# Optimization experiments

Measured on AMD Instinct MI355X. Metric: run time of the kernel, lower is better.

## Reference

```python
import jax, jax.numpy as jnp
import numpy as np

N_NODES = 50000
N_EDGES = 600000
IN_DIM = 64
HIDDEN = 128
N_REL = 10
N_LAYERS = 6
N_GRAPHS = 64
LN_EPS = 1e-5


def setup_inputs() -> dict:
    key = jax.random.key(0)
    ks = jax.random.split(key, 12)
    x = jax.random.normal(ks[0], (N_NODES, IN_DIM), dtype=jnp.float32)
    edge_index = jax.random.randint(ks[1], (2, N_EDGES), 0, N_NODES, dtype=jnp.int32)
    edge_type = jax.random.randint(ks[2], (N_EDGES,), 0, N_REL, dtype=jnp.int32)
    batch = jnp.sort(jax.random.randint(ks[3], (N_NODES,), 0, N_GRAPHS, dtype=jnp.int32))
    s_in = 1.0 / np.sqrt(IN_DIM)
    s_h = 1.0 / np.sqrt(HIDDEN)
    Wp = jax.random.uniform(ks[4], (IN_DIM, HIDDEN), jnp.float32, -s_in, s_in)
    bp = jax.random.uniform(ks[5], (HIDDEN,), jnp.float32, -s_in, s_in)
    rel_w = jax.random.uniform(ks[6], (N_LAYERS, N_REL, HIDDEN, HIDDEN), jnp.float32, -s_h, s_h)
    root_w = jax.random.uniform(ks[7], (N_LAYERS, HIDDEN, HIDDEN), jnp.float32, -s_h, s_h)
    conv_b = jnp.zeros((N_LAYERS, HIDDEN), jnp.float32)
    ln_g = jnp.ones((N_LAYERS, HIDDEN), jnp.float32)
    ln_b = jnp.zeros((N_LAYERS, HIDDEN), jnp.float32)
    return {"x": x, "edge_index": edge_index, "edge_type": edge_type, "batch": batch,
            "Wp": Wp, "bp": bp, "rel_w": rel_w, "root_w": root_w, "conv_b": conv_b,
            "ln_g": ln_g, "ln_b": ln_b}


def _layer_norm(h, g, b):
    mu = jnp.mean(h, axis=-1, keepdims=True)
    var = jnp.mean(jnp.square(h - mu), axis=-1, keepdims=True)
    return (h - mu) * jax.lax.rsqrt(var + LN_EPS) * g + b


def _rgcn_conv(h, src, dst, etype, Wr, Wroot, b):
    # PyG RGCNConv (aggr='mean'): out_i = x_i @ root + bias + sum_r mean_{j in N_r(i)} x_j @ W_r
    out = h @ Wroot + b
    hs = h[src]  # [E, H] gathered messages (relation-agnostic, transform after aggregation)
    for r in range(N_REL):
        m = (etype == r)
        msg = jnp.where(m[:, None], hs, 0.0)
        s = jax.ops.segment_sum(msg, dst, num_segments=N_NODES)
        cnt = jax.ops.segment_sum(m.astype(h.dtype), dst, num_segments=N_NODES)
        agg = s / jnp.maximum(cnt, 1.0)[:, None]
        out = out + agg @ Wr[r]
    return out


def reference(x, edge_index, edge_type, batch, Wp, bp, rel_w, root_w, conv_b, ln_g, ln_b):
    src, dst = edge_index[0], edge_index[1]
    h = x @ Wp + bp
    for l in range(N_LAYERS):
        residual = h
        h = _rgcn_conv(h, src, dst, edge_type, rel_w[l], root_w[l], conv_b[l])
        h = _layer_norm(h, ln_g[l], ln_b[l])
        h = jax.nn.relu(h)
        # dropout: identity in eval mode
        h = h + residual
    return jax.ops.segment_sum(h, batch, num_segments=N_GRAPHS)  # global_add_pool -> [G, H]
```

## Files before the change

kernel.cpp:

```cpp
#include <hip/hip_runtime.h>

#define NN 50000
#define NE 600000
#define IND 64
#define HID 128
#define NREL 10
#define NLAY 6
#define NG 64
#define LN_EPS 1e-5f
#define NMAT 11

typedef __attribute__((ext_vector_type(8))) short bf8;
typedef __attribute__((ext_vector_type(4))) float f4;

__device__ __forceinline__ ushort f2bf(float x) {
  uint u = __float_as_uint(x);
  u += 0x7fff + ((u >> 16) & 1);
  return (ushort)(u >> 16);
}
__device__ __forceinline__ float bf2f(ushort h) {
  return __uint_as_float(((uint)h) << 16);
}

__global__ void zero_kernel(float* __restrict__ p, int n) {
  int i = blockIdx.x * blockDim.x + threadIdx.x;
  int stride = gridDim.x * blockDim.x;
  for (; i < n; i += stride) p[i] = 0.f;
}

__global__ void count_edges(const int* __restrict__ dst, const int* __restrict__ et,
                            float* __restrict__ winv, int* __restrict__ deg) {
  int e = blockIdx.x * 256 + threadIdx.x;
  if (e >= NE) return;
  int d = dst[e];
  atomicAdd(&winv[d * NREL + et[e]], 1.0f);
  atomicAdd(&deg[d], 1);
}

__global__ void invert_winv(float* __restrict__ winv) {
  int i = blockIdx.x * 256 + threadIdx.x;
  if (i < NN * NREL) winv[i] = 1.0f / fmaxf(winv[i], 1.0f);
}

__global__ void scan_block(const int* __restrict__ deg, int* __restrict__ rowstart,
                           int* __restrict__ partial) {
  __shared__ int sh[256];
  int i = blockIdx.x * 256 + threadIdx.x;
  int v = (i < NN) ? deg[i] : 0;
  sh[threadIdx.x] = v;
  __syncthreads();
  int x = v;
  for (int off = 1; off < 256; off <<= 1) {
    int y = (threadIdx.x >= off) ? sh[threadIdx.x - off] : 0;
    __syncthreads();
    x += y;
    sh[threadIdx.x] = x;
    __syncthreads();
  }
  if (i < NN) rowstart[i] = x - v;
  if (threadIdx.x == 255) partial[blockIdx.x] = x;
}

__global__ void scan_partials(int* __restrict__ partial, int nb) {
  __shared__ int sh[256];
  int v = (threadIdx.x < nb) ? partial[threadIdx.x] : 0;
  sh[threadIdx.x] = v;
  __syncthreads();
  int x = v;
  for (int off = 1; off < 256; off <<= 1) {
    int y = (threadIdx.x >= off) ? sh[threadIdx.x - off] : 0;
    __syncthreads();
    x += y;
    sh[threadIdx.x] = x;
    __syncthreads();
  }
  partial[threadIdx.x] = x - v;
}

__global__ void scan_add(int* __restrict__ rowstart, const int* __restrict__ partial) {
  int i = blockIdx.x * 256 + threadIdx.x;
  if (i < NN) rowstart[i] += partial[i >> 8];
  if (i == 0) rowstart[NN] = NE;
}

__global__ void fill_csr(const int* __restrict__ dst, const int* __restrict__ src,
                         const int* __restrict__ et, int* __restrict__ fillpos,
                         const int* __restrict__ rowstart, const float* __restrict__ winv,
                         int* __restrict__ pkd, float* __restrict__ wsc) {
  int e = blockIdx.x * 256 + threadIdx.x;
  if (e >= NE) return;
  int d = dst[e], t = et[e];
  int pos = rowstart[d] + atomicAdd(&fillpos[d], 1);
  pkd[pos] = (src[e] << 4) | t;
  wsc[pos] = winv[d * NREL + t];
}

__global__ void transpose_split_frag(const float* __restrict__ src, ushort* __restrict__ dh,
                                     ushort* __restrict__ dl, int nmat, int K,
                                     int ddiv, int dmul, int dadd) {
  int i = blockIdx.x * 256 + threadIdx.x;
  int tot = nmat * K * 128;
  if (i >= tot) return;
  int m = i / (K * 128);
  int rem = i - m * (K * 128);
  int k = rem / 128;
  int n = rem - k * 128;
  float v = src[i];
  ushort h = f2bf(v);
  int dm = (m / ddiv) * dmul + (m % ddiv) + dadd;
  size_t o = (size_t)dm * (K * 128) + (size_t)(n >> 4) * (K * 16) + (k >> 3) * 128 +
             (n & 15) * 8 + (k & 7);
  dh[o] = h;
  dl[o] = f2bf(v - bf2f(h));
}

template <int K>
__global__ __launch_bounds__(256) void split_frag(const float* __restrict__ src,
                                                  ushort* __restrict__ dh,
                                                  ushort* __restrict__ dl) {
  constexpr int TOT = 16 * K;
  __shared__ ushort sh[TOT], sl[TOT];
  int grp = blockIdx.x;
  const float* s = src + (size_t)grp * TOT;
  for (int i = threadIdx.x * 4; i < TOT; i += 1024) {
    float4 v = *(const float4*)(s + i);
    int nl = i / K, d = i - nl * K;
    int off = (d >> 3) * 128 + nl * 8 + (d & 7);
    ushort h0 = f2bf(v.x), h1 = f2bf(v.y), h2 = f2bf(v.z), h3 = f2bf(v.w);
    *(uint*)(sh + off) = (uint)h0 | ((uint)h1 << 16);
    *(uint*)(sh + off + 2) = (uint)h2 | ((uint)h3 << 16);
    *(uint*)(sl + off) = (uint)f2bf(v.x - bf2f(h0)) | ((uint)f2bf(v.y - bf2f(h1)) << 16);
    *(uint*)(sl + off + 2) = (uint)f2bf(v.z - bf2f(h2)) | ((uint)f2bf(v.w - bf2f(h3)) << 16);
  }
  __syncthreads();
  size_t base = (size_t)grp * TOT;
  for (int i = threadIdx.x * 8; i < TOT; i += 2048) {
    *(bf8*)(dh + base + i) = *(const bf8*)(sh + i);
    *(bf8*)(dl + base + i) = *(const bf8*)(sl + i);
  }
}

struct Frags {
  bf8 ah[4], al[4], bh[4], bl[4];
};

template <int K>
__device__ __forceinline__ void load_frags(Frags& f, int ks, const ushort* Abh,
                                           const ushort* Abl, const ushort* Bbh,
                                           const ushort* Bbl) {
#pragma unroll
  for (int m = 0; m < 4; ++m) {
    f.ah[m] = *(const bf8*)(Abh + (size_t)m * (K * 16) + ks * 512);
    f.al[m] = *(const bf8*)(Abl + (size_t)m * (K * 16) + ks * 512);
  }
#pragma unroll
  for (int n = 0; n < 4; ++n) {
    f.bh[n] = *(const bf8*)(Bbh + (size_t)n * (K * 16) + ks * 512);
    f.bl[n] = *(const bf8*)(Bbl + (size_t)n * (K * 16) + ks * 512);
  }
}

__device__ __forceinline__ void mfma_frags(f4 (&acc)[4][4], const Frags& f) {
#pragma unroll
  for (int m = 0; m < 4; ++m)
#pragma unroll
    for (int n = 0; n < 4; ++n) {
      acc[m][n] = __builtin_amdgcn_mfma_f32_16x16x32_bf16(f.ah[m], f.bh[n], acc[m][n], 0, 0, 0);
      acc[m][n] = __builtin_amdgcn_mfma_f32_16x16x32_bf16(f.al[m], f.bh[n], acc[m][n], 0, 0, 0);
      acc[m][n] = __builtin_amdgcn_mfma_f32_16x16x32_bf16(f.ah[m], f.bl[n], acc[m][n], 0, 0, 0);
    }
}

template <int K>
__global__ __launch_bounds__(256) void gemm_frag(
    const ushort* __restrict__ Ah, const ushort* __restrict__ Al,
    const ushort* __restrict__ Bh, const ushort* __restrict__ Bl,
    const float* __restrict__ bias, float* __restrict__ Cf, ushort* __restrict__ Cb,
    int ldc, int M, int nrel) {
  int nwg = gridDim.x * gridDim.y;
  int lin = blockIdx.y * gridDim.x + blockIdx.x;
  int q = nwg >> 3, r8 = nwg & 7;
  int xcd = lin & 7, sub = lin >> 3;
  int swz = (xcd < r8) ? (xcd * (q + 1) + sub) : (r8 * (q + 1) + (xcd - r8) * q + sub);
  int bx = swz % gridDim.x;
  int by = swz / gridDim.x;

  const int bm = by * 128;
  const int tid = threadIdx.x, w = tid >> 6, lane = tid & 63;
  const int wr = (w >> 1) * 64, wc = (w & 1) * 64;
  const int lr = lane & 15;

  const ushort* Abh = Ah + ((size_t)(bm >> 4) + (wr >> 4)) * (K * 16) + lane * 8;
  const ushort* Abl = Al + ((size_t)(bm >> 4) + (wr >> 4)) * (K * 16) + lane * 8;
  const ushort* Bbh = Bh + (size_t)bx * (128 * K) + (size_t)(wc >> 4) * (K * 16) + lane * 8;
  const ushort* Bbl = Bl + (size_t)bx * (128 * K) + (size_t)(wc >> 4) * (K * 16) + lane * 8;

  f4 acc[4][4] = {};
  Frags fa, fb;
  if constexpr (K == 64) {
    load_frags<K>(fa, 0, Abh, Abl, Bbh, Bbl);
    load_frags<K>(fb, 1, Abh, Abl, Bbh, Bbl);
    mfma_frags(acc, fa);
    mfma_frags(acc, fb);
  } else {
    load_frags<K>(fa, 0, Abh, Abl, Bbh, Bbl);
    load_frags<K>(fb, 1, Abh, Abl, Bbh, Bbl);
    mfma_frags(acc, fa);
    load_frags<K>(fa, 2, Abh, Abl, Bbh, Bbl);
    mfma_frags(acc, fb);
    load_frags<K>(fb, 3, Abh, Abl, Bbh, Bbl);
    mfma_frags(acc, fa);
    mfma_frags(acc, fb);
  }

  const bool isroot = (bx == nrel);
  const int rgrp = (lane >> 4) * 4;
#pragma unroll
  for (int n = 0; n < 4; ++n) {
    int col = wc + n * 16 + lr;
    float bv = isroot ? bias[col] : 0.f;
#pragma unroll
    for (int m = 0; m < 4; ++m) {
      int r0 = bm + wr + m * 16 + rgrp;
#pragma unroll
      for (int j = 0; j < 4; ++j) {
        int r = r0 + j;
        if (r < M) {
          float v = acc[m][n][j];
          if (isroot) Cf[(size_t)r * 128 + col] = v + bv;
          else Cb[(size_t)r * ldc + bx * 128 + col] = f2bf(v);
        }
      }
    }
  }
}

__global__ __launch_bounds__(256) void aggregate(
    const int* __restrict__ pkd, const float* __restrict__ wsc,
    const int* __restrict__ rowstart, const ushort* __restrict__ T,
    float* __restrict__ OUT, int r0, int G) {
  int node = blockIdx.x * 4 + (threadIdx.x >> 6);
  if (node >= NN) return;
  int lane = threadIdx.x & 63;
  int e0 = rowstart[node], e1 = rowstart[node + 1];
  const int TW = G * HID;
  const int lo = lane * 2;
  float ax = 0.f, ay = 0.f;
  int p = e0;
  constexpr int U = 8;
  for (; p + U <= e1; p += U) {
    int pk[U];
    float wg[U];
    size_t ad[U];
#pragma unroll
    for (int u = 0; u < U; ++u) {
      pk[u] = pkd[p + u];
      wg[u] = wsc[p + u];
    }
#pragma unroll
    for (int u = 0; u < U; ++u) {
      int t = (pk[u] & 15) - r0;
      bool ok = (unsigned)t < (unsigned)G;
      ad[u] = ok ? ((size_t)(pk[u] >> 4) * TW + t * HID) : 0;
      if (!ok) wg[u] = 0.f;
    }
    uint v[U];
#pragma unroll
    for (int u = 0; u < U; ++u) v[u] = *(const uint*)(T + ad[u] + lo);
#pragma unroll
    for (int u = 0; u < U; ++u) {
      ax += wg[u] * bf2f((ushort)(v[u] & 0xffffu));
      ay += wg[u] * bf2f((ushort)(v[u] >> 16));
    }
  }
  for (; p < e1; ++p) {
    int pk = pkd[p];
    float wg = wsc[p];
    int t = (pk & 15) - r0;
    if ((unsigned)t < (unsigned)G) {
      uint v = *(const uint*)(T + (size_t)(pk >> 4) * TW + t * HID + lo);
      ax += wg * bf2f((ushort)(v & 0xffffu));
      ay += wg * bf2f((ushort)(v >> 16));
    }
  }
  float2* o = (float2*)(OUT + (size_t)node * HID + lo);
  float2 cur = *o;
  cur.x += ax;
  cur.y += ay;
  *o = cur;
}

__global__ __launch_bounds__(256) void ln_relu_res_frag(
    const float* __restrict__ OUT, float* __restrict__ h,
    const float* __restrict__ g, const float* __restrict__ b,
    ushort* __restrict__ dh, ushort* __restrict__ dl) {
  __shared__ ushort sh[2048], sl[2048];
  int grp = blockIdx.x;
  int w = threadIdx.x >> 6, lane = threadIdx.x & 63;
  float2 gg = *(const float2*)(g + lane * 2);
  float2 bb = *(const float2*)(b + lane * 2);
#pragma unroll
  for (int p = 0; p < 4; ++p) {
    int r = w * 4 + p;
    int node = grp * 16 + r;
    float2 v = *(const float2*)(OUT + (size_t)node * HID + lane * 2);
    float s = v.x + v.y, sq = v.x * v.x + v.y * v.y;
#pragma unroll
    for (int off = 32; off; off >>= 1) {
      s += __shfl_xor(s, off);
      sq += __shfl_xor(sq, off);
    }
    float mu = s * (1.f / HID);
    float var = sq * (1.f / HID) - mu * mu;
    float rs = rsqrtf(var + LN_EPS);
    float2 rr = *(const float2*)(h + (size_t)node * HID + lane * 2);
    float y0 = fmaxf((v.x - mu) * rs * gg.x + bb.x, 0.f) + rr.x;
    float y1 = fmaxf((v.y - mu) * rs * gg.y + bb.y, 0.f) + rr.y;
    *(float2*)(h + (size_t)node * HID + lane * 2) = make_float2(y0, y1);
    int d = lane * 2;
    int off2 = (d >> 3) * 128 + r * 8 + (d & 7);
    ushort h0 = f2bf(y0), h1 = f2bf(y1);
    *(uint*)(sh + off2) = (uint)h0 | ((uint)h1 << 16);
    *(uint*)(sl + off2) =
        (uint)f2bf(y0 - bf2f(h0)) | ((uint)f2bf(y1 - bf2f(h1)) << 16);
  }
  __syncthreads();
  size_t base = (size_t)grp * 2048;
  int t8 = threadIdx.x * 8;
  *(bf8*)(dh + base + t8) = *(const bf8*)(sh + t8);
  *(bf8*)(dl + base + t8) = *(const bf8*)(sl + t8);
}

__global__ void pool_kernel(const float* __restrict__ h, const int* __restrict__ batch,
                            float* __restrict__ out) {
  int n0 = blockIdx.x * 64;
  if (n0 >= NN) return;
  int t = threadIdx.x;
  int nend = min(n0 + 64, NN);
  int cur = batch[n0];
  float acc = 0.f;
  for (int n = n0; n < nend; ++n) {
    int gph = batch[n];
    if (gph != cur) {
      atomicAdd(&out[cur * HID + t], acc);
      acc = 0.f;
      cur = gph;
    }
    acc += h[(size_t)n * HID + t];
  }
  atomicAdd(&out[cur * HID + t], acc);
}

extern "C" void kernel_launch(void* const* d_in, const int* in_sizes, int n_in,
                              void* d_out, int out_size, void* d_ws, size_t ws_size,
                              hipStream_t stream) {
  const float* x = (const float*)d_in[0];
  const int* ei = (const int*)d_in[1];
  const int* et = (const int*)d_in[2];
  const int* batch = (const int*)d_in[3];
  const float* Wp = (const float*)d_in[4];
  const float* bp = (const float*)d_in[5];
  const float* rel_w = (const float*)d_in[6];
  const float* root_w = (const float*)d_in[7];
  const float* conv_b = (const float*)d_in[8];
  const float* ln_g = (const float*)d_in[9];
  const float* ln_b = (const float*)d_in[10];
  float* out = (float*)d_out;
  const int* srcv = ei;
  const int* dstv = ei + NE;

  const int NGRP = NN / 16;
  const int NGRP_PAD = NGRP + 3;

  char* w = (char*)d_ws;
  auto alloc = [&](size_t bytes) {
    char* p = w;
    w += (bytes + 255) & ~(size_t)255;
    return p;
  };
  float* h = (float*)alloc((size_t)NN * HID * 4);
  float* OUT = (float*)alloc((size_t)NN * HID * 4);
  float* winv = (float*)alloc((size_t)NN * NREL * 4);
  int* deg = (int*)alloc((size_t)NN * 4);
  int* rowstart = (int*)alloc((size_t)(NN + 1) * 4);
  int* fillpos = (int*)alloc((size_t)NN * 4);
  int* pkd = (int*)alloc((size_t)NE * 4);
  float* wsc = (float*)alloc((size_t)NE * 4);
  int* partial = (int*)alloc(256 * 4);
  ushort* xh = (ushort*)alloc((size_t)NGRP_PAD * 1024 * 2);
  ushort* xl = (ushort*)alloc((size_t)NGRP_PAD * 1024 * 2);
  ushort* hh = (ushort*)alloc((size_t)NGRP_PAD * 2048 * 2);
  ushort* hl = (ushort*)alloc((size_t)NGRP_PAD * 2048 * 2);
  ushort* Wph = (ushort*)alloc((size_t)IND * HID * 2);
  ushort* Wpl = (ushort*)alloc((size_t)IND * HID * 2);
  ushort* Relh = (ushort*)alloc((size_t)NLAY * NMAT * HID * HID * 2);
  ushort* Rell = (ushort*)alloc((size_t)NLAY * NMAT * HID * HID * 2);

  size_t used = (size_t)(w - (char*)d_ws);
  size_t rem = (ws_size > used) ? ws_size - used : 0;
  int G = 1;
  if (rem >= (size_t)NN * 10 * HID * 2) G = 10;
  else if (rem >= (size_t)NN * 5 * HID * 2) G = 5;
  else if (rem >= (size_t)NN * 2 * HID * 2) G = 2;
  ushort* T = (ushort*)alloc((size_t)NN * G * HID * 2);
  const int P = NREL / G;

  const int NB_E = (NE + 255) / 256;
  const int NB_N = (NN + 255) / 256;
  const int MB = (NN + 127) / 128;

  zero_kernel<<<dim3(512), dim3(256), 0, stream>>>(winv, NN * NREL);
  zero_kernel<<<dim3(256), dim3(256), 0, stream>>>((float*)deg, NN);
  zero_kernel<<<dim3(256), dim3(256), 0, stream>>>((float*)fillpos, NN);
  zero_kernel<<<dim3(32), dim3(256), 0, stream>>>(out, NG * HID);

  count_edges<<<dim3(NB_E), dim3(256), 0, stream>>>(dstv, et, winv, deg);
  invert_winv<<<dim3((NN * NREL + 255) / 256), dim3(256), 0, stream>>>(winv);
  scan_block<<<dim3(NB_N), dim3(256), 0, stream>>>(deg, rowstart, partial);
  scan_partials<<<dim3(1), dim3(256), 0, stream>>>(partial, NB_N);
  scan_add<<<dim3(NB_N), dim3(256), 0, stream>>>(rowstart, partial);
  fill_csr<<<dim3(NB_E), dim3(256), 0, stream>>>(dstv, srcv, et, fillpos, rowstart,
                                                 winv, pkd, wsc);

  transpose_split_frag<<<dim3((IND * HID + 255) / 256), dim3(256), 0, stream>>>(
      Wp, Wph, Wpl, 1, IND, 1, 1, 0);
  transpose_split_frag<<<dim3((NLAY * NREL * HID * HID + 255) / 256), dim3(256), 0, stream>>>(
      rel_w, Relh, Rell, NLAY * NREL, HID, NREL, NMAT, 0);
  transpose_split_frag<<<dim3((NLAY * HID * HID + 255) / 256), dim3(256), 0, stream>>>(
      root_w, Relh, Rell, NLAY, HID, 1, NMAT, NREL);

  split_frag<IND><<<dim3(NGRP), dim3(256), 0, stream>>>(x, xh, xl);

  gemm_frag<IND><<<dim3(1, MB), dim3(256), 0, stream>>>(
      xh, xl, Wph, Wpl, bp, h, (ushort*)nullptr, 128, NN, 0);
  split_frag<HID><<<dim3(NGRP), dim3(256), 0, stream>>>(h, hh, hl);

  for (int l = 0; l < NLAY; ++l) {
    const ushort* Bh = Relh + (size_t)l * NMAT * HID * HID;
    const ushort* Bl = Rell + (size_t)l * NMAT * HID * HID;
    if (G == NREL) {
      gemm_frag<HID><<<dim3(NREL + 1, MB), dim3(256), 0, stream>>>(
          hh, hl, Bh, Bl, conv_b + (size_t)l * HID, OUT, T, G * HID, NN, NREL);
      aggregate<<<dim3(NN / 4), dim3(256), 0, stream>>>(pkd, wsc, rowstart, T, OUT, 0, G);
    } else {
      gemm_frag<HID><<<dim3(1, MB), dim3(256), 0, stream>>>(
          hh, hl, Bh + (size_t)NREL * HID * HID, Bl + (size_t)NREL * HID * HID,
          conv_b + (size_t)l * HID, OUT, (ushort*)nullptr, 128, NN, 0);
      for (int p = 0; p < P; ++p) {
        gemm_frag<HID><<<dim3(G, MB), dim3(256), 0, stream>>>(
            hh, hl, Bh + (size_t)p * G * HID * HID, Bl + (size_t)p * G * HID * HID,
            (const float*)nullptr, (float*)nullptr, T, G * HID, NN, -1);
        aggregate<<<dim3(NN / 4), dim3(256), 0, stream>>>(pkd, wsc, rowstart, T, OUT,
                                                          p * G, G);
      }
    }
    ln_relu_res_frag<<<dim3(NGRP), dim3(256), 0, stream>>>(
        OUT, h, ln_g + (size_t)l * HID, ln_b + (size_t)l * HID, hh, hl);
  }

  pool_kernel<<<dim3((NN + 63) / 64), dim3(128), 0, stream>>>(h, batch, out);
}
```

Baseline: 1.084 ms.

## Fuse aggregation with layernorm and stage GEMM bf16 output through LDS

Adds an agg_ln kernel that performs the neighbour aggregation and the layernorm/relu/residual in one pass. This avoids writing OUT back to memory and launching a separate LN kernel, and it skips the split write on the last layer. The GEMM epilogue for relation outputs now stages bf16 tiles in shared memory so the global stores are coalesced 16-byte writes. The three zero kernels are also merged into one launch over the contiguous buffer. The costs are 34KB of LDS per GEMM block, which may lower occupancy, and one aggregation block per 16 nodes instead of per 4.

```diff
diff --git a/kernel.cpp b/kernel.cpp
--- a/kernel.cpp
+++ b/kernel.cpp
@@ -177,6 +177,7 @@
     const ushort* __restrict__ Bh, const ushort* __restrict__ Bl,
     const float* __restrict__ bias, float* __restrict__ Cf, ushort* __restrict__ Cb,
     int ldc, int M, int nrel) {
+  __shared__ ushort st[128][136];
   int nwg = gridDim.x * gridDim.y;
   int lin = blockIdx.y * gridDim.x + blockIdx.x;
   int q = nwg >> 3, r8 = nwg & 7;
@@ -213,25 +214,120 @@
     mfma_frags(acc, fb);
   }
 
-  const bool isroot = (bx == nrel);
   const int rgrp = (lane >> 4) * 4;
-#pragma unroll
-  for (int n = 0; n < 4; ++n) {
-    int col = wc + n * 16 + lr;
-    float bv = isroot ? bias[col] : 0.f;
-#pragma unroll
-    for (int m = 0; m < 4; ++m) {
-      int r0 = bm + wr + m * 16 + rgrp;
-#pragma unroll
-      for (int j = 0; j < 4; ++j) {
-        int r = r0 + j;
-        if (r < M) {
-          float v = acc[m][n][j];
-          if (isroot) Cf[(size_t)r * 128 + col] = v + bv;
-          else Cb[(size_t)r * ldc + bx * 128 + col] = f2bf(v);
+  if (bx == nrel) {
+#pragma unroll
+    for (int n = 0; n < 4; ++n) {
+      int col = wc + n * 16 + lr;
+      float bv = bias[col];
+#pragma unroll
+      for (int m = 0; m < 4; ++m) {
+        int r0 = bm + wr + m * 16 + rgrp;
+#pragma unroll
+        for (int j = 0; j < 4; ++j) {
+          int r = r0 + j;
+          if (r < M) Cf[(size_t)r * 128 + col] = acc[m][n][j] + bv;
         }
       }
     }
+  } else {
+#pragma unroll
+    for (int n = 0; n < 4; ++n) {
+      int col = wc + n * 16 + lr;
+#pragma unroll
+      for (int m = 0; m < 4; ++m) {
+        int r0 = wr + m * 16 + rgrp;
+#pragma unroll
+        for (int j = 0; j < 4; ++j) st[r0 + j][col] = f2bf(acc[m][n][j]);
+      }
+    }
+    __syncthreads();
+    const int rr = tid >> 4;
+    const int cc = (tid & 15) * 8;
+#pragma unroll
+    for (int it = 0; it < 8; ++it) {
+      int row = it * 16 + rr;
+      int grow = bm + row;
+      if (grow < M) {
+        bf8 v = *(const bf8*)&st[row][cc];
+        *(bf8*)(Cb + (size_t)grow * ldc + bx * 128 + cc) = v;
+      }
+    }
+  }
+}
+
+__global__ __launch_bounds__(256) void agg_ln(
+    const int* __restrict__ pkd, const float* __restrict__ wsc,
+    const int* __restrict__ rowstart, const ushort* __restrict__ T,
+    const float* __restrict__ OUT, float* __restrict__ h,
+    const float* __restrict__ g, const float* __restrict__ b,
+    ushort* __restrict__ dh, ushort* __restrict__ dl, int writeSplit) {
+  __shared__ ushort sh[2048], sl[2048];
+  const int grp = blockIdx.x;
+  const int w = threadIdx.x >> 6, lane = threadIdx.x & 63;
+  const int lo = lane * 2;
+  float2 gg = *(const float2*)(g + lo);
+  float2 bb = *(const float2*)(b + lo);
+  constexpr int TW = NREL * HID;
+#pragma unroll
+  for (int p4 = 0; p4 < 4; ++p4) {
+    int r = w * 4 + p4;
+    int node = grp * 16 + r;
+    float2 rt = *(const float2*)(OUT + (size_t)node * HID + lo);
+    float ax = 0.f, ay = 0.f;
+    int e0 = rowstart[node], e1 = rowstart[node + 1];
+    int p = e0;
+    constexpr int U = 8;
+    for (; p + U <= e1; p += U) {
+      int pk[U];
+      float wg[U];
+      uint v[U];
+#pragma unroll
+      for (int u = 0; u < U; ++u) {
+        pk[u] = pkd[p + u];
+        wg[u] = wsc[p + u];
+      }
+#pragma unroll
+      for (int u = 0; u < U; ++u)
+        v[u] = *(const uint*)(T + (size_t)(pk[u] >> 4) * TW + (pk[u] & 15) * HID + lo);
+#pragma unroll
+      for (int u = 0; u < U; ++u) {
+        ax += wg[u] * bf2f((ushort)(v[u] & 0xffffu));
+        ay += wg[u] * bf2f((ushort)(v[u] >> 16));
+      }
+    }
+    for (; p < e1; ++p) {
+      int pk = pkd[p];
+      float wg = wsc[p];
+      uint v = *(const uint*)(T + (size_t)(pk >> 4) * TW + (pk & 15) * HID + lo);
+      ax += wg * bf2f((ushort)(v & 0xffffu));
+      ay += wg * bf2f((ushort)(v >> 16));
+    }
+    float vx = rt.x + ax, vy = rt.y + ay;
+    float s = vx + vy, sq = vx * vx + vy * vy;
+#pragma unroll
+    for (int off = 32; off; off >>= 1) {
+      s += __shfl_xor(s, off);
+      sq += __shfl_xor(sq, off);
+    }
+    float mu = s * (1.f / HID);
+    float var = sq * (1.f / HID) - mu * mu;
+    float rs = rsqrtf(var + LN_EPS);
+    float2 rr2 = *(const float2*)(h + (size_t)node * HID + lo);
+    float y0 = fmaxf((vx - mu) * rs * gg.x + bb.x, 0.f) + rr2.x;
+    float y1 = fmaxf((vy - mu) * rs * gg.y + bb.y, 0.f) + rr2.y;
+    *(float2*)(h + (size_t)node * HID + lo) = make_float2(y0, y1);
+    int off2 = (lo >> 3) * 128 + r * 8 + (lo & 7);
+    ushort h0 = f2bf(y0), h1 = f2bf(y1);
+    *(uint*)(sh + off2) = (uint)h0 | ((uint)h1 << 16);
+    *(uint*)(sl + off2) = (uint)f2bf(y0 - bf2f(h0)) | ((uint)f2bf(y1 - bf2f(h1)) << 16);
+  }
+  __syncthreads();
+  if (writeSplit) {
+    size_t base = (size_t)grp * 2048;
+    int t8 = threadIdx.x * 8;
+    *(bf8*)(dh + base + t8) = *(const bf8*)(sh + t8);
+    *(bf8*)(dl + base + t8) = *(const bf8*)(sl + t8);
   }
 }
 
@@ -321,8 +417,7 @@
     int off2 = (d >> 3) * 128 + r * 8 + (d & 7);
     ushort h0 = f2bf(y0), h1 = f2bf(y1);
     *(uint*)(sh + off2) = (uint)h0 | ((uint)h1 << 16);
-    *(uint*)(sl + off2) =
-        (uint)f2bf(y0 - bf2f(h0)) | ((uint)f2bf(y1 - bf2f(h1)) << 16);
+    *(uint*)(sl + off2) = (uint)f2bf(y0 - bf2f(h0)) | ((uint)f2bf(y1 - bf2f(h1)) << 16);
   }
   __syncthreads();
   size_t base = (size_t)grp * 2048;
@@ -384,6 +479,7 @@
   int* deg = (int*)alloc((size_t)NN * 4);
   int* rowstart = (int*)alloc((size_t)(NN + 1) * 4);
   int* fillpos = (int*)alloc((size_t)NN * 4);
+  char* zend = w;
   int* pkd = (int*)alloc((size_t)NE * 4);
   float* wsc = (float*)alloc((size_t)NE * 4);
   int* partial = (int*)alloc(256 * 4);
@@ -408,10 +504,9 @@
   const int NB_E = (NE + 255) / 256;
   const int NB_N = (NN + 255) / 256;
   const int MB = (NN + 127) / 128;
-
-  zero_kernel<<<dim3(512), dim3(256), 0, stream>>>(winv, NN * NREL);
-  zero_kernel<<<dim3(256), dim3(256), 0, stream>>>((float*)deg, NN);
-  zero_kernel<<<dim3(256), dim3(256), 0, stream>>>((float*)fillpos, NN);
+  const int ZSPAN = (int)((zend - (char*)winv) / 4);
+
+  zero_kernel<<<dim3(1024), dim3(256), 0, stream>>>(winv, ZSPAN);
   zero_kernel<<<dim3(32), dim3(256), 0, stream>>>(out, NG * HID);
 
   count_edges<<<dim3(NB_E), dim3(256), 0, stream>>>(dstv, et, winv, deg);
@@ -441,7 +536,9 @@
     if (G == NREL) {
       gemm_frag<HID><<<dim3(NREL + 1, MB), dim3(256), 0, stream>>>(
           hh, hl, Bh, Bl, conv_b + (size_t)l * HID, OUT, T, G * HID, NN, NREL);
-      aggregate<<<dim3(NN / 4), dim3(256), 0, stream>>>(pkd, wsc, rowstart, T, OUT, 0, G);
+      agg_ln<<<dim3(NGRP), dim3(256), 0, stream>>>(
+          pkd, wsc, rowstart, T, OUT, h, ln_g + (size_t)l * HID, ln_b + (size_t)l * HID,
+          hh, hl, (l != NLAY - 1) ? 1 : 0);
     } else {
       gemm_frag<HID><<<dim3(1, MB), dim3(256), 0, stream>>>(
           hh, hl, Bh + (size_t)NREL * HID * HID, Bl + (size_t)NREL * HID * HID,
@@ -453,9 +550,9 @@
         aggregate<<<dim3(NN / 4), dim3(256), 0, stream>>>(pkd, wsc, rowstart, T, OUT,
                                                           p * G, G);
       }
-    }
-    ln_relu_res_frag<<<dim3(NGRP), dim3(256), 0, stream>>>(
-        OUT, h, ln_g + (size_t)l * HID, ln_b + (size_t)l * HID, hh, hl);
+      ln_relu_res_frag<<<dim3(NGRP), dim3(256), 0, stream>>>(
+          OUT, h, ln_g + (size_t)l * HID, ln_b + (size_t)l * HID, hh, hl);
+    }
   }
 
   pool_kernel<<<dim3((NN + 63) / 64), dim3(128), 0, stream>>>(h, batch, out);
```

New measurement: 909.4 us. 16.1% less time.

## Aggregate per-relation features before transform and fuse into one K=1536 GEMM

Applied to the files above, without the earlier changes.

Swaps the order of work: each layer now gathers bf16 node features per relation (mean-weighted) into a per-node 10x128 buffer, then runs one GEMM with concatenated K (root hi, root lo, 10 relation blocks) against a prepacked weight matrix. The old path computed ten per-relation transforms for every node and then gathered from that large transformed table. The new order removes the large intermediate T write and read and the multiple launches. In exchange the aggregated messages are bf16 with no low-part correction, and the root term drops the lo-by-lo product, which may cost accuracy. It also merges the zeroing launches and skips the split writes on the last layer.

```diff
diff --git a/kernel.cpp b/kernel.cpp
--- a/kernel.cpp
+++ b/kernel.cpp
@@ -8,7 +8,6 @@
 #define NLAY 6
 #define NG 64
 #define LN_EPS 1e-5f
-#define NMAT 11
 
 typedef __attribute__((ext_vector_type(8))) short bf8;
 typedef __attribute__((ext_vector_type(4))) float f4;
@@ -96,28 +95,54 @@
 }
 
 __global__ void transpose_split_frag(const float* __restrict__ src, ushort* __restrict__ dh,
-                                     ushort* __restrict__ dl, int nmat, int K,
-                                     int ddiv, int dmul, int dadd) {
+                                     ushort* __restrict__ dl, int K) {
   int i = blockIdx.x * 256 + threadIdx.x;
-  int tot = nmat * K * 128;
+  int tot = K * 128;
   if (i >= tot) return;
-  int m = i / (K * 128);
-  int rem = i - m * (K * 128);
-  int k = rem / 128;
-  int n = rem - k * 128;
+  int k = i / 128;
+  int n = i - k * 128;
   float v = src[i];
   ushort h = f2bf(v);
-  int dm = (m / ddiv) * dmul + (m % ddiv) + dadd;
-  size_t o = (size_t)dm * (K * 128) + (size_t)(n >> 4) * (K * 16) + (k >> 3) * 128 +
-             (n & 15) * 8 + (k & 7);
+  size_t o = (size_t)(n >> 4) * (K * 16) + (k >> 3) * 128 + (n & 15) * 8 + (k & 7);
   dh[o] = h;
   dl[o] = f2bf(v - bf2f(h));
+}
+
+__global__ void pack_B(const float* __restrict__ root_w, const float* __restrict__ rel_w,
+                       ushort* __restrict__ Bp) {
+  int i = blockIdx.x * 256 + threadIdx.x;
+  const int tot = NLAY * 1536 * 128;
+  if (i >= tot) return;
+  int l = i / (1536 * 128);
+  int rem = i - l * (1536 * 128);
+  int k = rem >> 7;
+  int n = rem & 127;
+  ushort s1, s2;
+  if (k < 128) {
+    float v = root_w[(size_t)l * 16384 + k * 128 + n];
+    s1 = f2bf(v);
+    s2 = f2bf(v - bf2f(s1));
+  } else if (k < 256) {
+    float v = root_w[(size_t)l * 16384 + (k - 128) * 128 + n];
+    s1 = f2bf(v);
+    s2 = 0;
+  } else {
+    int r = (k - 256) >> 7, kk = (k - 256) & 127;
+    float v = rel_w[(((size_t)l * NREL + r) * 128 + kk) * 128 + n];
+    s1 = f2bf(v);
+    s2 = f2bf(v - bf2f(s1));
+  }
+  size_t off = (size_t)(n >> 4) * 24576 + (k >> 3) * 128 + (n & 15) * 8 + (k & 7);
+  size_t base = (size_t)l * 2 * 196608;
+  Bp[base + off] = s1;
+  Bp[base + 196608 + off] = s2;
 }
 
 template <int K>
 __global__ __launch_bounds__(256) void split_frag(const float* __restrict__ src,
                                                   ushort* __restrict__ dh,
-                                                  ushort* __restrict__ dl) {
+                                                  ushort* __restrict__ dl,
+                                                  ushort* __restrict__ db) {
   constexpr int TOT = 16 * K;
   __shared__ ushort sh[TOT], sl[TOT];
   int grp = blockIdx.x;
@@ -131,6 +156,12 @@
     *(uint*)(sh + off + 2) = (uint)h2 | ((uint)h3 << 16);
     *(uint*)(sl + off) = (uint)f2bf(v.x - bf2f(h0)) | ((uint)f2bf(v.y - bf2f(h1)) << 16);
     *(uint*)(sl + off + 2) = (uint)f2bf(v.z - bf2f(h2)) | ((uint)f2bf(v.w - bf2f(h3)) << 16);
+    if (db) {
+      uint2 pk;
+      pk.x = (uint)h0 | ((uint)h1 << 16);
+      pk.y = (uint)h2 | ((uint)h3 << 16);
+      *(uint2*)(db + (size_t)(grp * 16 + nl) * K + d) = pk;
+    }
   }
   __syncthreads();
   size_t base = (size_t)grp * TOT;
@@ -175,135 +206,193 @@
 __global__ __launch_bounds__(256) void gemm_frag(
     const ushort* __restrict__ Ah, const ushort* __restrict__ Al,
     const ushort* __restrict__ Bh, const ushort* __restrict__ Bl,
-    const float* __restrict__ bias, float* __restrict__ Cf, ushort* __restrict__ Cb,
-    int ldc, int M, int nrel) {
-  int nwg = gridDim.x * gridDim.y;
-  int lin = blockIdx.y * gridDim.x + blockIdx.x;
-  int q = nwg >> 3, r8 = nwg & 7;
-  int xcd = lin & 7, sub = lin >> 3;
-  int swz = (xcd < r8) ? (xcd * (q + 1) + sub) : (r8 * (q + 1) + (xcd - r8) * q + sub);
-  int bx = swz % gridDim.x;
-  int by = swz / gridDim.x;
-
-  const int bm = by * 128;
+    const float* __restrict__ bias, float* __restrict__ Cf, int M) {
+  const int bm = blockIdx.y * 128;
   const int tid = threadIdx.x, w = tid >> 6, lane = tid & 63;
   const int wr = (w >> 1) * 64, wc = (w & 1) * 64;
   const int lr = lane & 15;
 
   const ushort* Abh = Ah + ((size_t)(bm >> 4) + (wr >> 4)) * (K * 16) + lane * 8;
   const ushort* Abl = Al + ((size_t)(bm >> 4) + (wr >> 4)) * (K * 16) + lane * 8;
-  const ushort* Bbh = Bh + (size_t)bx * (128 * K) + (size_t)(wc >> 4) * (K * 16) + lane * 8;
-  const ushort* Bbl = Bl + (size_t)bx * (128 * K) + (size_t)(wc >> 4) * (K * 16) + lane * 8;
+  const ushort* Bbh = Bh + (size_t)(wc >> 4) * (K * 16) + lane * 8;
+  const ushort* Bbl = Bl + (size_t)(wc >> 4) * (K * 16) + lane * 8;
 
   f4 acc[4][4] = {};
   Frags fa, fb;
-  if constexpr (K == 64) {
-    load_frags<K>(fa, 0, Abh, Abl, Bbh, Bbl);
-    load_frags<K>(fb, 1, Abh, Abl, Bbh, Bbl);
-    mfma_frags(acc, fa);
-    mfma_frags(acc, fb);
-  } else {
-    load_frags<K>(fa, 0, Abh, Abl, Bbh, Bbl);
-    load_frags<K>(fb, 1, Abh, Abl, Bbh, Bbl);
-    mfma_frags(acc, fa);
-    load_frags<K>(fa, 2, Abh, Abl, Bbh, Bbl);
-    mfma_frags(acc, fb);
-    load_frags<K>(fb, 3, Abh, Abl, Bbh, Bbl);
-    mfma_frags(acc, fa);
-    mfma_frags(acc, fb);
-  }
-
-  const bool isroot = (bx == nrel);
+  load_frags<K>(fa, 0, Abh, Abl, Bbh, Bbl);
+  load_frags<K>(fb, 1, Abh, Abl, Bbh, Bbl);
+  mfma_frags(acc, fa);
+  mfma_frags(acc, fb);
+
   const int rgrp = (lane >> 4) * 4;
 #pragma unroll
   for (int n = 0; n < 4; ++n) {
     int col = wc + n * 16 + lr;
-    float bv = isroot ? bias[col] : 0.f;
+    float bv = bias[col];
 #pragma unroll
     for (int m = 0; m < 4; ++m) {
       int r0 = bm + wr + m * 16 + rgrp;
 #pragma unroll
       for (int j = 0; j < 4; ++j) {
         int r = r0 + j;
-        if (r < M) {
-          float v = acc[m][n][j];
-          if (isroot) Cf[(size_t)r * 128 + col] = v + bv;
-          else Cb[(size_t)r * ldc + bx * 128 + col] = f2bf(v);
+        if (r < M) Cf[(size_t)r * 128 + col] = acc[m][n][j] + bv;
+      }
+    }
+  }
+}
+
+__global__ __launch_bounds__(256) void agg2(
+    const int* __restrict__ pkd, const float* __restrict__ wsc,
+    const int* __restrict__ rowstart, const ushort* __restrict__ hb,
+    ushort* __restrict__ AGG) {
+  __shared__ ushort st[16][1288];
+  const int grp = blockIdx.x;
+  const int w = threadIdx.x >> 6, lane = threadIdx.x & 63;
+#pragma unroll
+  for (int p4 = 0; p4 < 4; ++p4) {
+    const int row = w * 4 + p4;
+    const int node = grp * 16 + row;
+    float ac[NREL][2];
+#pragma unroll
+    for (int r = 0; r < NREL; ++r) {
+      ac[r][0] = 0.f;
+      ac[r][1] = 0.f;
+    }
+    const int e1 = rowstart[node + 1];
+    int p = rowstart[node];
+    constexpr int U = 8;
+    for (; p + U <= e1; p += U) {
+      int pk[U];
+      float wg[U];
+      uint v[U];
+#pragma unroll
+      for (int u = 0; u < U; ++u) {
+        pk[u] = pkd[p + u];
+        wg[u] = wsc[p + u];
+      }
+#pragma unroll
+      for (int u = 0; u < U; ++u)
+        v[u] = *(const uint*)(hb + (size_t)(pk[u] >> 4) * HID + lane * 2);
+#pragma unroll
+      for (int u = 0; u < U; ++u) {
+        float vx = wg[u] * bf2f((ushort)(v[u] & 0xffffu));
+        float vy = wg[u] * bf2f((ushort)(v[u] >> 16));
+        int t = pk[u] & 15;
+#pragma unroll
+        for (int r = 0; r < NREL; ++r) {
+          if (t == r) {
+            ac[r][0] += vx;
+            ac[r][1] += vy;
+          }
         }
       }
     }
-  }
-}
-
-__global__ __launch_bounds__(256) void aggregate(
-    const int* __restrict__ pkd, const float* __restrict__ wsc,
-    const int* __restrict__ rowstart, const ushort* __restrict__ T,
-    float* __restrict__ OUT, int r0, int G) {
-  int node = blockIdx.x * 4 + (threadIdx.x >> 6);
-  if (node >= NN) return;
-  int lane = threadIdx.x & 63;
-  int e0 = rowstart[node], e1 = rowstart[node + 1];
-  const int TW = G * HID;
-  const int lo = lane * 2;
-  float ax = 0.f, ay = 0.f;
-  int p = e0;
-  constexpr int U = 8;
-  for (; p + U <= e1; p += U) {
-    int pk[U];
-    float wg[U];
-    size_t ad[U];
-#pragma unroll
-    for (int u = 0; u < U; ++u) {
-      pk[u] = pkd[p + u];
-      wg[u] = wsc[p + u];
-    }
-#pragma unroll
-    for (int u = 0; u < U; ++u) {
-      int t = (pk[u] & 15) - r0;
-      bool ok = (unsigned)t < (unsigned)G;
-      ad[u] = ok ? ((size_t)(pk[u] >> 4) * TW + t * HID) : 0;
-      if (!ok) wg[u] = 0.f;
-    }
-    uint v[U];
-#pragma unroll
-    for (int u = 0; u < U; ++u) v[u] = *(const uint*)(T + ad[u] + lo);
-#pragma unroll
-    for (int u = 0; u < U; ++u) {
-      ax += wg[u] * bf2f((ushort)(v[u] & 0xffffu));
-      ay += wg[u] * bf2f((ushort)(v[u] >> 16));
-    }
-  }
-  for (; p < e1; ++p) {
-    int pk = pkd[p];
-    float wg = wsc[p];
-    int t = (pk & 15) - r0;
-    if ((unsigned)t < (unsigned)G) {
-      uint v = *(const uint*)(T + (size_t)(pk >> 4) * TW + t * HID + lo);
-      ax += wg * bf2f((ushort)(v & 0xffffu));
-      ay += wg * bf2f((ushort)(v >> 16));
-    }
-  }
-  float2* o = (float2*)(OUT + (size_t)node * HID + lo);
-  float2 cur = *o;
-  cur.x += ax;
-  cur.y += ay;
-  *o = cur;
-}
-
-__global__ __launch_bounds__(256) void ln_relu_res_frag(
+    for (; p < e1; ++p) {
+      int pk = pkd[p];
+      float wg = wsc[p];
+      uint v = *(const uint*)(hb + (size_t)(pk >> 4) * HID + lane * 2);
+      float vx = wg * bf2f((ushort)(v & 0xffffu));
+      float vy = wg * bf2f((ushort)(v >> 16));
+      int t = pk & 15;
+#pragma unroll
+      for (int r = 0; r < NREL; ++r) {
+        if (t == r) {
+          ac[r][0] += vx;
+          ac[r][1] += vy;
+        }
+      }
+    }
+#pragma unroll
+    for (int r = 0; r < NREL; ++r)
+      *(uint*)&st[row][r * HID + lane * 2] =
+          (uint)f2bf(ac[r][0]) | ((uint)f2bf(ac[r][1]) << 16);
+  }
+  __syncthreads();
+  size_t base = (size_t)grp * 20480;
+#pragma unroll
+  for (int it = 0; it < 10; ++it) {
+    int o = it * 2048 + threadIdx.x * 8;
+    int chunk = o >> 7, rw = (o >> 3) & 15;
+    *(bf8*)(AGG + base + o) = *(const bf8*)&st[rw][chunk * 8];
+  }
+}
+
+__device__ __forceinline__ void g2_step(f4 (&acc)[2][4], const ushort* Ap, size_t mstride,
+                                        int aoff, const ushort* B1, const ushort* B2,
+                                        int boff) {
+  bf8 a[2], b1[4], b2[4];
+#pragma unroll
+  for (int m = 0; m < 2; ++m) a[m] = *(const bf8*)(Ap + m * mstride + aoff);
+#pragma unroll
+  for (int n = 0; n < 4; ++n) {
+    b1[n] = *(const bf8*)(B1 + n * 24576 + boff);
+    b2[n] = *(const bf8*)(B2 + n * 24576 + boff);
+  }
+#pragma unroll
+  for (int m = 0; m < 2; ++m)
+#pragma unroll
+    for (int n = 0; n < 4; ++n) {
+      acc[m][n] = __builtin_amdgcn_mfma_f32_16x16x32_bf16(a[m], b1[n], acc[m][n], 0, 0, 0);
+      acc[m][n] = __builtin_amdgcn_mfma_f32_16x16x32_bf16(a[m], b2[n], acc[m][n], 0, 0, 0);
+    }
+}
+
+__global__ __launch_bounds__(256) void gemm2(
+    const ushort* __restrict__ Ahh, const ushort* __restrict__ Ahl,
+    const ushort* __restrict__ AGG, const ushort* __restrict__ Bp,
+    const float* __restrict__ bias, float* __restrict__ OUT, int M) {
+  const int bm = blockIdx.x * 64;
+  const int tid = threadIdx.x, w = tid >> 6, lane = tid & 63;
+  const int wrg = (w >> 1) * 2;
+  const int wc = (w & 1) * 64;
+  const int agrp = (bm >> 4) + wrg;
+  const ushort* pA0 = Ahh + (size_t)agrp * 2048 + lane * 8;
+  const ushort* pA1 = Ahl + (size_t)agrp * 2048 + lane * 8;
+  const ushort* pA2 = AGG + (size_t)agrp * 20480 + lane * 8;
+  const ushort* pB1 = Bp + (size_t)(wc >> 4) * 24576 + lane * 8;
+  const ushort* pB2 = pB1 + 196608;
+
+  f4 acc[2][4] = {};
+#pragma unroll
+  for (int ks = 0; ks < 4; ++ks) g2_step(acc, pA0, 2048, ks * 512, pB1, pB2, ks * 512);
+#pragma unroll
+  for (int ks = 0; ks < 4; ++ks) g2_step(acc, pA1, 2048, ks * 512, pB1, pB2, (4 + ks) * 512);
+#pragma unroll
+  for (int ks = 0; ks < 40; ++ks) g2_step(acc, pA2, 20480, ks * 512, pB1, pB2, (8 + ks) * 512);
+
+  const int rgrp = (lane >> 4) * 4;
+#pragma unroll
+  for (int n = 0; n < 4; ++n) {
+    int col = wc + n * 16 + (lane & 15);
+    float bv = bias[col];
+#pragma unroll
+    for (int m = 0; m < 2; ++m) {
+      int r0 = bm + (wrg + m) * 16 + rgrp;
+#pragma unroll
+      for (int j = 0; j < 4; ++j) {
+        int r = r0 + j;
+        if (r < M) OUT[(size_t)r * 128 + col] = acc[m][n][j] + bv;
+      }
+    }
+  }
+}
+
+__global__ __launch_bounds__(256) void ln2(
     const float* __restrict__ OUT, float* __restrict__ h,
     const float* __restrict__ g, const float* __restrict__ b,
-    ushort* __restrict__ dh, ushort* __restrict__ dl) {
+    ushort* __restrict__ dh, ushort* __restrict__ dl, ushort* __restrict__ db,
+    int writeSplit) {
   __shared__ ushort sh[2048], sl[2048];
   int grp = blockIdx.x;
   int w = threadIdx.x >> 6, lane = threadIdx.x & 63;
-  float2 gg = *(const float2*)(g + lane * 2);
-  float2 bb = *(const float2*)(b + lane * 2);
+  int lo = lane * 2;
+  float2 gg = *(const float2*)(g + lo);
+  float2 bb = *(const float2*)(b + lo);
 #pragma unroll
   for (int p = 0; p < 4; ++p) {
     int r = w * 4 + p;
     int node = grp * 16 + r;
-    float2 v = *(const float2*)(OUT + (size_t)node * HID + lane * 2);
+    float2 v = *(const float2*)(OUT + (size_t)node * HID + lo);
     float s = v.x + v.y, sq = v.x * v.x + v.y * v.y;
 #pragma unroll
     for (int off = 32; off; off >>= 1) {
@@ -313,22 +402,25 @@
     float mu = s * (1.f / HID);
     float var = sq * (1.f / HID) - mu * mu;
     float rs = rsqrtf(var + LN_EPS);
-    float2 rr = *(const float2*)(h + (size_t)node * HID + lane * 2);
+    float2 rr = *(const float2*)(h + (size_t)node * HID + lo);
     float y0 = fmaxf((v.x - mu) * rs * gg.x + bb.x, 0.f) + rr.x;
     float y1 = fmaxf((v.y - mu) * rs * gg.y + bb.y, 0.f) + rr.y;
-    *(float2*)(h + (size_t)node * HID + lane * 2) = make_float2(y0, y1);
-    int d = lane * 2;
-    int off2 = (d >> 3) * 128 + r * 8 + (d & 7);
-    ushort h0 = f2bf(y0), h1 = f2bf(y1);
-    *(uint*)(sh + off2) = (uint)h0 | ((uint)h1 << 16);
-    *(uint*)(sl + off2) =
-        (uint)f2bf(y0 - bf2f(h0)) | ((uint)f2bf(y1 - bf2f(h1)) << 16);
+    *(float2*)(h + (size_t)node * HID + lo) = make_float2(y0, y1);
+    if (writeSplit) {
+      ushort h0 = f2bf(y0), h1 = f2bf(y1);
+      int off2 = (lo >> 3) * 128 + r * 8 + (lo & 7);
+      *(uint*)(sh + off2) = (uint)h0 | ((uint)h1 << 16);
+      *(uint*)(sl + off2) = (uint)f2bf(y0 - bf2f(h0)) | ((uint)f2bf(y1 - bf2f(h1)) << 16);
+      *(uint*)(db + (size_t)node * HID + lo) = (uint)h0 | ((uint)h1 << 16);
+    }
   }
   __syncthreads();
-  size_t base = (size_t)grp * 2048;
-  int t8 = threadIdx.x * 8;
-  *(bf8*)(dh + base + t8) = *(const bf8*)(sh + t8);
-  *(bf8*)(dl + base + t8) = *(const bf8*)(sl + t8);
+  if (writeSplit) {
+    size_t base = (size_t)grp * 2048;
+    int t8 = threadIdx.x * 8;
+    *(bf8*)(dh + base + t8) = *(const bf8*)(sh + t8);
+    *(bf8*)(dl + base + t8) = *(const bf8*)(sl + t8);
+  }
 }
 
 __global__ void pool_kernel(const float* __restrict__ h, const int* __restrict__ batch,
@@ -384,6 +476,7 @@
   int* deg = (int*)alloc((size_t)NN * 4);
   int* rowstart = (int*)alloc((size_t)(NN + 1) * 4);
   int* fillpos = (int*)alloc((size_t)NN * 4);
+  char* zend = w;
   int* pkd = (int*)alloc((size_t)NE * 4);
   float* wsc = (float*)alloc((size_t)NE * 4);
   int* partial = (int*)alloc(256 * 4);
@@ -391,27 +484,19 @@
   ushort* xl = (ushort*)alloc((size_t)NGRP_PAD * 1024 * 2);
   ushort* hh = (ushort*)alloc((size_t)NGRP_PAD * 2048 * 2);
   ushort* hl = (ushort*)alloc((size_t)NGRP_PAD * 2048 * 2);
+  ushort* hb = (ushort*)alloc((size_t)NN * HID * 2);
   ushort* Wph = (ushort*)alloc((size_t)IND * HID * 2);
   ushort* Wpl = (ushort*)alloc((size_t)IND * HID * 2);
-  ushort* Relh = (ushort*)alloc((size_t)NLAY * NMAT * HID * HID * 2);
-  ushort* Rell = (ushort*)alloc((size_t)NLAY * NMAT * HID * HID * 2);
-
-  size_t used = (size_t)(w - (char*)d_ws);
-  size_t rem = (ws_size > used) ? ws_size - used : 0;
-  int G = 1;
-  if (rem >= (size_t)NN * 10 * HID * 2) G = 10;
-  else if (rem >= (size_t)NN * 5 * HID * 2) G = 5;
-  else if (rem >= (size_t)NN * 2 * HID * 2) G = 2;
-  ushort* T = (ushort*)alloc((size_t)NN * G * HID * 2);
-  const int P = NREL / G;
+  ushort* Bp = (ushort*)alloc((size_t)NLAY * 2 * 196608 * 2);
+  ushort* AGG = (ushort*)alloc((size_t)NGRP_PAD * 20480 * 2);
 
   const int NB_E = (NE + 255) / 256;
   const int NB_N = (NN + 255) / 256;
   const int MB = (NN + 127) / 128;
-
-  zero_kernel<<<dim3(512), dim3(256), 0, stream>>>(winv, NN * NREL);
-  zero_kernel<<<dim3(256), dim3(256), 0, stream>>>((float*)deg, NN);
-  zero_kernel<<<dim3(256), dim3(256), 0, stream>>>((float*)fillpos, NN);
+  const int MB2 = (NN + 63) / 64;
+  const int ZSPAN = (int)((zend - (char*)winv) / 4);
+
+  zero_kernel<<<dim3(1024), dim3(256), 0, stream>>>(winv, ZSPAN);
   zero_kernel<<<dim3(32), dim3(256), 0, stream>>>(out, NG * HID);
 
   count_edges<<<dim3(NB_E), dim3(256), 0, stream>>>(dstv, et, winv, deg);
@@ -423,39 +508,22 @@
                                                  winv, pkd, wsc);
 
   transpose_split_frag<<<dim3((IND * HID + 255) / 256), dim3(256), 0, stream>>>(
-      Wp, Wph, Wpl, 1, IND, 1, 1, 0);
-  transpose_split_frag<<<dim3((NLAY * NREL * HID * HID + 255) / 256), dim3(256), 0, stream>>>(
-      rel_w, Relh, Rell, NLAY * NREL, HID, NREL, NMAT, 0);
-  transpose_split_frag<<<dim3((NLAY * HID * HID + 255) / 256), dim3(256), 0, stream>>>(
-      root_w, Relh, Rell, NLAY, HID, 1, NMAT, NREL);
-
-  split_frag<IND><<<dim3(NGRP), dim3(256), 0, stream>>>(x, xh, xl);
-
-  gemm_frag<IND><<<dim3(1, MB), dim3(256), 0, stream>>>(
-      xh, xl, Wph, Wpl, bp, h, (ushort*)nullptr, 128, NN, 0);
-  split_frag<HID><<<dim3(NGRP), dim3(256), 0, stream>>>(h, hh, hl);
+      Wp, Wph, Wpl, IND);
+  pack_B<<<dim3((NLAY * 1536 * 128 + 255) / 256), dim3(256), 0, stream>>>(
+      root_w, rel_w, Bp);
+
+  split_frag<IND><<<dim3(NGRP), dim3(256), 0, stream>>>(x, xh, xl, (ushort*)nullptr);
+
+  gemm_frag<IND><<<dim3(1, MB), dim3(256), 0, stream>>>(xh, xl, Wph, Wpl, bp, h, NN);
+  split_frag<HID><<<dim3(NGRP), dim3(256), 0, stream>>>(h, hh, hl, hb);
 
   for (int l = 0; l < NLAY; ++l) {
-    const ushort* Bh = Relh + (size_t)l * NMAT * HID * HID;
-    const ushort* Bl = Rell + (size_t)l * NMAT * HID * HID;
-    if (G == NREL) {
-      gemm_frag<HID><<<dim3(NREL + 1, MB), dim3(256), 0, stream>>>(
-          hh, hl, Bh, Bl, conv_b + (size_t)l * HID, OUT, T, G * HID, NN, NREL);
-      aggregate<<<dim3(NN / 4), dim3(256), 0, stream>>>(pkd, wsc, rowstart, T, OUT, 0, G);
-    } else {
-      gemm_frag<HID><<<dim3(1, MB), dim3(256), 0, stream>>>(
-          hh, hl, Bh + (size_t)NREL * HID * HID, Bl + (size_t)NREL * HID * HID,
-          conv_b + (size_t)l * HID, OUT, (ushort*)nullptr, 128, NN, 0);
-      for (int p = 0; p < P; ++p) {
-        gemm_frag<HID><<<dim3(G, MB), dim3(256), 0, stream>>>(
-            hh, hl, Bh + (size_t)p * G * HID * HID, Bl + (size_t)p * G * HID * HID,
-            (const float*)nullptr, (float*)nullptr, T, G * HID, NN, -1);
-        aggregate<<<dim3(NN / 4), dim3(256), 0, stream>>>(pkd, wsc, rowstart, T, OUT,
-                                                          p * G, G);
-      }
-    }
-    ln_relu_res_frag<<<dim3(NGRP), dim3(256), 0, stream>>>(
-        OUT, h, ln_g + (size_t)l * HID, ln_b + (size_t)l * HID, hh, hl);
+    agg2<<<dim3(NGRP), dim3(256), 0, stream>>>(pkd, wsc, rowstart, hb, AGG);
+    gemm2<<<dim3(MB2), dim3(256), 0, stream>>>(
+        hh, hl, AGG, Bp + (size_t)l * 2 * 196608, conv_b + (size_t)l * HID, OUT, NN);
+    ln2<<<dim3(NGRP), dim3(256), 0, stream>>>(
+        OUT, h, ln_g + (size_t)l * HID, ln_b + (size_t)l * HID, hh, hl, hb,
+        (l != NLAY - 1) ? 1 : 0);
   }
 
   pool_kernel<<<dim3((NN + 63) / 64), dim3(128), 0, stream>>>(h, batch, out);
```

Result: slower. 1.384 ms (+27.6%).
